# Performance work log

Hardware: AMD Instinct MI355X
Metric: run time of the kernel (lower is better)

The kernel has to match this reference:

```python
import jax, jax.numpy as jnp
import numpy as np

B, S, D, H = 4, 2048, 1024, 16
DH = D // H
NEG = -10000.0


def setup_inputs() -> dict:
    key = jax.random.key(0)
    ks = jax.random.split(key, 12)
    scale = 0.02
    inp = {
        "q": jax.random.normal(ks[0], (B, S, D), jnp.float32),
        "k": jax.random.normal(ks[1], (B, S, D), jnp.float32),
        "v": jax.random.normal(ks[2], (B, S, D), jnp.float32),
        "mask": jnp.triu(jnp.ones((S, S), jnp.bool_), k=1),  # True = masked (causal)
        "Wq": jax.random.normal(ks[3], (D, D), jnp.float32) * scale,
        "bq": jnp.zeros((D,), jnp.float32),
        "Wk": jax.random.normal(ks[4], (D, D), jnp.float32) * scale,
        "bk": jnp.zeros((D,), jnp.float32),
        "Wv": jax.random.normal(ks[5], (D, D), jnp.float32) * scale,
        "bv": jnp.zeros((D,), jnp.float32),
        "Wo": jax.random.normal(ks[6], (D, D), jnp.float32) * scale,
        "bo": jnp.zeros((D,), jnp.float32),
    }
    return inp


def _split(x):
    # [B,S,D] -> [B,H,S,DH]
    return x.reshape(B, S, H, DH).transpose(0, 2, 1, 3)


def reference(q, k, v, mask, Wq, bq, Wk, bk, Wv, bv, Wo, bo):
    # torch Linear: y = x @ W.T + b
    qh = _split(q @ Wq.T + bq)
    kh = _split(k @ Wk.T + bk)
    vh = _split(v @ Wv.T + bv)
    # scaled dot-product scores: [B,H,S,S]
    scores = jnp.einsum("bhqd,bhkd->bhqk", qh, kh) / jnp.sqrt(jnp.float32(DH))
    scores = scores + jnp.where(mask, jnp.float32(NEG), jnp.float32(0.0))
    attn = jax.nn.softmax(scores, axis=-1)  # dropout_rate=0 -> identity
    out = jnp.einsum("bhqk,bhkd->bhqd", attn, vh)
    out = out.transpose(0, 2, 1, 3).reshape(B, S, D)
    return out @ Wo.T + bo
```

## Files before the change

### kernel.cpp

```cpp
#include <hip/hip_runtime.h>
#include <hip/hip_bf16.h>


#define B_ 4
#define S_ 2048
#define D_ 1024
#define H_ 16
#define DH_ 64
#define M_ (B_*S_)
#define MASKADD (-14427.0f)
#define QSCALE  (0.180336880f)

typedef __attribute__((ext_vector_type(8)))  __bf16 bf16x8;
typedef __attribute__((ext_vector_type(8)))  unsigned short ushort8;
typedef __attribute__((ext_vector_type(4)))  float f32x4;
typedef __attribute__((ext_vector_type(16))) float f32x16;

__device__ __forceinline__ unsigned short f2bf(float f) {
  __hip_bfloat16 h = __float2bfloat16(f);
  union { __hip_bfloat16 h; unsigned short u; } c; c.h = h; return c.u;
}

__device__ __forceinline__ f32x4 mfma16(bf16x8 a, bf16x8 b, f32x4 c) {
  return __builtin_amdgcn_mfma_f32_16x16x32_bf16(a, b, c, 0, 0, 0);
}
__device__ __forceinline__ f32x16 mfma32(bf16x8 a, bf16x8 b, f32x16 c) {
  return __builtin_amdgcn_mfma_f32_32x32x16_bf16(a, b, c, 0, 0, 0);
}

__device__ __forceinline__ unsigned cvtpk(float lo, float hi) {
  unsigned r;
  asm("v_cvt_pk_bf16_f32 %0, %1, %2" : "=v"(r) : "v"(lo), "v"(hi));
  return r;
}

__device__ __forceinline__ void gld_lds16(const void* g, void* l) {
  __builtin_amdgcn_global_load_lds(
      (const __attribute__((address_space(1))) unsigned int*)g,
      (__attribute__((address_space(3))) unsigned int*)l, 16, 0, 0);
}

__global__ void cvt3_kernel(const float* __restrict__ p0, const float* __restrict__ p1,
                            const float* __restrict__ p2,
                            unsigned short* __restrict__ o0, unsigned short* __restrict__ o1,
                            unsigned short* __restrict__ o2, int n4) {
  int i = blockIdx.x * blockDim.x + threadIdx.x;
  if (i >= n4) return;
  const float* in = (blockIdx.y == 0) ? p0 : (blockIdx.y == 1 ? p1 : p2);
  unsigned short* out = (blockIdx.y == 0) ? o0 : (blockIdx.y == 1 ? o1 : o2);
  float4 f = reinterpret_cast<const float4*>(in)[i];
  ushort4 o;
  o.x = f2bf(f.x); o.y = f2bf(f.y); o.z = f2bf(f.z); o.w = f2bf(f.w);
  reinterpret_cast<ushort4*>(out)[i] = o;
}

__global__ void cvt4_kernel(const float* __restrict__ p0, const float* __restrict__ p1,
                            const float* __restrict__ p2, const float* __restrict__ p3,
                            unsigned short* __restrict__ o0, unsigned short* __restrict__ o1,
                            unsigned short* __restrict__ o2, unsigned short* __restrict__ o3,
                            int n4) {
  int i = blockIdx.x * blockDim.x + threadIdx.x;
  if (i >= n4) return;
  const float* in  = (blockIdx.y == 0) ? p0 : (blockIdx.y == 1 ? p1 : (blockIdx.y == 2 ? p2 : p3));
  unsigned short* out = (blockIdx.y == 0) ? o0 : (blockIdx.y == 1 ? o1 : (blockIdx.y == 2 ? o2 : o3));
  float4 f = reinterpret_cast<const float4*>(in)[i];
  ushort4 o;
  o.x = f2bf(f.x); o.y = f2bf(f.y); o.z = f2bf(f.z); o.w = f2bf(f.w);
  reinterpret_cast<ushort4*>(out)[i] = o;
}

__device__ __forceinline__
void gemm_body(const unsigned short* __restrict__ A, const unsigned short* __restrict__ W,
               const float* __restrict__ bias, void* __restrict__ outp,
               int mode, bool sc,
               unsigned short (*sA)[128*32], unsigned short (*sB)[128*32])
{
  const int tid  = threadIdx.x;
  const int lane = tid & 63, wid = tid >> 6;
  const int bx = blockIdx.x;
  const int j8 = bx & 7, i8 = bx >> 3;
  const int mt = j8*8 + (i8 >> 3), nt = i8 & 7;
  const int m0 = mt*128, n0 = nt*128;
  const int wr = wid >> 1, wc = wid & 1;

  f32x4 acc[4][4];
  #pragma unroll
  for (int i = 0; i < 4; ++i)
    #pragma unroll
    for (int j = 0; j < 4; ++j)
      #pragma unroll
      for (int r = 0; r < 4; ++r) acc[i][j][r] = 0.0f;

  auto stage = [&](int bufi, int kt) {
    const unsigned short* Ab = A + (size_t)m0*D_ + kt*32;
    const unsigned short* Wb = W + (size_t)n0*D_ + kt*32;
    #pragma unroll
    for (int p = 0; p < 2; ++p) {
      int r = 32*wid + 16*p + (lane >> 2);
      int c = (lane & 3) * 8;
      gld_lds16(Ab + (size_t)r*D_ + c, &sA[bufi][(32*wid + 16*p)*32]);
      gld_lds16(Wb + (size_t)r*D_ + c, &sB[bufi][(32*wid + 16*p)*32]);
    }
  };

  stage(0, 0);
  int buf = 0;
  for (int kt = 0; kt < D_/32; ++kt) {
    __syncthreads();
    if (kt + 1 < D_/32) stage(buf ^ 1, kt + 1);
    bf16x8 aF[4], bF[4];
    #pragma unroll
    for (int i = 0; i < 4; ++i)
      aF[i] = *(const bf16x8*)&sA[buf][(64*wr + 16*i + (lane & 15))*32 + (lane >> 4)*8];
    #pragma unroll
    for (int j = 0; j < 4; ++j)
      bF[j] = *(const bf16x8*)&sB[buf][(64*wc + 16*j + (lane & 15))*32 + (lane >> 4)*8];
    #pragma unroll
    for (int i = 0; i < 4; ++i)
      #pragma unroll
      for (int j = 0; j < 4; ++j)
        acc[i][j] = mfma16(aF[i], bF[j], acc[i][j]);
    buf ^= 1;
  }

  #pragma unroll
  for (int i = 0; i < 4; ++i) {
    int gr0 = m0 + 64*wr + 16*i + ((lane >> 4) << 2);
    #pragma unroll
    for (int j = 0; j < 4; ++j) {
      int gc = n0 + 64*wc + 16*j + (lane & 15);
      float bv = bias[gc];
      if (mode == 2) {
        int b = gr0 >> 11, s = gr0 & (S_ - 1);
        int hh = gc >> 6, dh = gc & (DH_ - 1);
        ushort4 o;
        o.x = f2bf(acc[i][j][0] + bv); o.y = f2bf(acc[i][j][1] + bv);
        o.z = f2bf(acc[i][j][2] + bv); o.w = f2bf(acc[i][j][3] + bv);
        *(ushort4*)&((unsigned short*)outp)[(((size_t)b*H_ + hh)*DH_ + dh)*S_ + s] = o;
      } else {
        #pragma unroll
        for (int r = 0; r < 4; ++r) {
          float v = acc[i][j][r] + bv;
          if (sc) v *= QSCALE;
          int gr = gr0 + r;
          if (mode == 0) {
            int b = gr >> 11, s = gr & (S_ - 1);
            int hh = gc >> 6, dh = gc & (DH_ - 1);
            ((unsigned short*)outp)[(((size_t)b*H_ + hh)*S_ + s)*DH_ + dh] = f2bf(v);
          } else {
            ((float*)outp)[(size_t)gr*D_ + gc] = v;
          }
        }
      }
    }
  }
}

__global__ __launch_bounds__(256, 2)
void gemm_qkv(const unsigned short* __restrict__ Aq, const unsigned short* __restrict__ Ak,
              const unsigned short* __restrict__ Av,
              const unsigned short* __restrict__ Wq_, const unsigned short* __restrict__ Wk_,
              const unsigned short* __restrict__ Wv_,
              const float* __restrict__ bq_, const float* __restrict__ bk_,
              const float* __restrict__ bv_,
              unsigned short* __restrict__ Oq, unsigned short* __restrict__ Ok,
              unsigned short* __restrict__ Ov)
{
  __shared__ unsigned short sA[2][128*32];
  __shared__ unsigned short sB[2][128*32];
  const int y = blockIdx.y;
  const unsigned short* A = (y == 0) ? Aq : (y == 1 ? Ak : Av);
  const unsigned short* W = (y == 0) ? Wq_ : (y == 1 ? Wk_ : Wv_);
  const float* bias        = (y == 0) ? bq_ : (y == 1 ? bk_ : bv_);
  unsigned short* outp     = (y == 0) ? Oq  : (y == 1 ? Ok  : Ov);
  gemm_body(A, W, bias, outp, (y == 2) ? 2 : 0, y == 0, sA, sB);
}

__global__ __launch_bounds__(256, 2)
void gemm_out(const unsigned short* __restrict__ A, const unsigned short* __restrict__ W,
              const float* __restrict__ bias, float* __restrict__ outp)
{
  __shared__ unsigned short sA[2][128*32];
  __shared__ unsigned short sB[2][128*32];
  gemm_body(A, W, bias, outp, 1, false, sA, sB);
}

__global__ __launch_bounds__(256)
void attn_kernel(const unsigned short* __restrict__ Qh, const unsigned short* __restrict__ Kh,
                 const unsigned short* __restrict__ Vt, unsigned short* __restrict__ AO)
{
  __shared__ unsigned short sK [2][64*64];
  __shared__ unsigned short sVt[2][64*64];

  const int tid = threadIdx.x, lane = tid & 63, wid = tid >> 6;
  const int l31 = lane & 31, h5 = lane >> 5;
  const int bh = blockIdx.x;
  const int chunk = 15 - (int)blockIdx.y;
  const int bb = bh >> 4, hd = bh & 15;
  const unsigned short* Qb = Qh + (size_t)bh * S_ * DH_;
  const unsigned short* Kb = Kh + (size_t)bh * S_ * DH_;
  const unsigned short* Vb = Vt + (size_t)bh * DH_ * S_;
  const int qc0 = chunk * 128;
  const int NT  = 2*chunk + 2;
  const int qw0 = qc0 + wid*32;
  const int q   = qw0 + l31;

  bf16x8 qF[4];
  #pragma unroll
  for (int c = 0; c < 4; ++c)
    qF[c] = *(const bf16x8*)(Qb + (size_t)q*DH_ + c*16 + h5*8);

  f32x16 zz;
  #pragma unroll
  for (int r = 0; r < 16; ++r) zz[r] = 0.0f;
  f32x16 accO0 = zz, accO1 = zz;
  float lsum = 0.0f;

  auto stageK = [&](int bufi, int t) {
    #pragma unroll
    for (int p = 0; p < 2; ++p) {
      int ch = 2*wid + p;
      int row = ch*8 + (lane >> 3);
      int cbs = ((lane & 7) * 16) ^ ((row & 7) << 4);
      gld_lds16(Kb + (size_t)(t*64 + row)*DH_ + (cbs >> 1), &sK[bufi][ch*512]);
    }
  };
  auto stageV = [&](int bufi, int t) {
    #pragma unroll
    for (int p = 0; p < 2; ++p) {
      int ch = 2*wid + p;
      int row = ch*8 + (lane >> 3);
      int cbs = ((lane & 7) * 16) ^ ((row & 7) << 4);
      gld_lds16(Vb + (size_t)row*S_ + t*64 + (cbs >> 1), &sVt[bufi][ch*512]);
    }
  };

  stageK(0, 0);
  stageV(0, 0);

  int buf = 0;
  for (int t = 0; t < NT; ++t) {
    __syncthreads();
    if (t + 1 < NT) { stageK(buf ^ 1, t + 1); stageV(buf ^ 1, t + 1); }

    #pragma unroll
    for (int sub = 0; sub < 2; ++sub) {
      const int kv0 = t*64 + sub*32;
      if (kv0 > qw0 + 31) continue;
      const bool dodiag = (kv0 + 31 > qw0);

      f32x16 st = zz;
      __builtin_amdgcn_s_setprio(1);
      #pragma unroll
      for (int c = 0; c < 4; ++c) {
        int row = sub*32 + l31;
        const char* base = (const char*)&sK[buf][0] + row*128;
        bf16x8 kf = *(const bf16x8*)(base + ((32*c + 16*h5) ^ ((row & 7) << 4)));
        st = mfma32(kf, qF[c], st);
      }
      __builtin_amdgcn_s_setprio(0);

      #pragma unroll
      for (int r = 0; r < 16; ++r) {
        float x = st[r];
        if (dodiag) {
          int kv = kv0 + (r & 3) + 8*(r >> 2) + 4*h5;
          if (kv > q) x += MASKADD;
        }
        x = __builtin_amdgcn_exp2f(x);
        st[r] = x;
        lsum += x;
      }

      #pragma unroll
      for (int hh = 0; hh < 2; ++hh) {
        union { unsigned u[4]; bf16x8 v; } pb;
        pb.u[0] = cvtpk(st[8*hh+0], st[8*hh+1]);
        pb.u[1] = cvtpk(st[8*hh+2], st[8*hh+3]);
        pb.u[2] = cvtpk(st[8*hh+4], st[8*hh+5]);
        pb.u[3] = cvtpk(st[8*hh+6], st[8*hh+7]);

        __builtin_amdgcn_s_setprio(1);
        #pragma unroll
        for (int dh = 0; dh < 2; ++dh) {
          int row = dh*32 + l31;
          const char* base = (const char*)&sVt[buf][0] + row*128;
          int sw = (row & 7) << 4;
          int X = 64*sub + 32*hh + 8*h5;
          union { uint2 g[2]; bf16x8 v; } vv;
          vv.g[0] = *(const uint2*)(base + ((X)      ^ sw));
          vv.g[1] = *(const uint2*)(base + ((X + 16) ^ sw));
          if (dh == 0) accO0 = mfma32(vv.v, pb.v, accO0);
          else         accO1 = mfma32(vv.v, pb.v, accO1);
        }
        __builtin_amdgcn_s_setprio(0);
      }
    }
    buf ^= 1;
  }

  float lt = lsum + __shfl_xor(lsum, 32, 64);
  float inv = 1.0f / lt;
  unsigned short* ao = AO + ((size_t)bb*S_ + q)*D_ + hd*DH_;
  #pragma unroll
  for (int dh = 0; dh < 2; ++dh) {
    const f32x16 A = dh ? accO1 : accO0;
    #pragma unroll
    for (int rq = 0; rq < 4; ++rq) {
      ushort4 o;
      o.x = f2bf(A[4*rq+0] * inv);
      o.y = f2bf(A[4*rq+1] * inv);
      o.z = f2bf(A[4*rq+2] * inv);
      o.w = f2bf(A[4*rq+3] * inv);
      int dbase = dh*32 + 8*rq + 4*h5;
      *(ushort4*)&ao[dbase] = o;
    }
  }
}

extern "C" void kernel_launch(void* const* d_in, const int* in_sizes, int n_in,
                              void* d_out, int out_size, void* d_ws, size_t ws_size,
                              hipStream_t stream)
{
  const float* q  = (const float*)d_in[0];
  const float* k  = (const float*)d_in[1];
  const float* v  = (const float*)d_in[2];
  const float* Wq = (const float*)d_in[4];
  const float* bq = (const float*)d_in[5];
  const float* Wk = (const float*)d_in[6];
  const float* bk = (const float*)d_in[7];
  const float* Wv = (const float*)d_in[8];
  const float* bv = (const float*)d_in[9];
  const float* Wo = (const float*)d_in[10];
  const float* bo = (const float*)d_in[11];

  unsigned short* ws = (unsigned short*)d_ws;
  const size_t MD = (size_t)M_ * D_;
  const size_t DD = (size_t)D_ * D_;
  unsigned short* qb  = ws;
  unsigned short* kb  = qb  + MD;
  unsigned short* vb  = kb  + MD;
  unsigned short* Wqb = vb  + MD;
  unsigned short* Wkb = Wqb + DD;
  unsigned short* Wvb = Wkb + DD;
  unsigned short* Wob = Wvb + DD;
  unsigned short* Qhb = Wob + DD;
  unsigned short* Khb = Qhb + MD;
  unsigned short* Vtb = Khb + MD;
  unsigned short* AOb = Vtb + MD;

  cvt3_kernel<<<dim3((int)(MD/4/256), 3), 256, 0, stream>>>(q, k, v, qb, kb, vb, (int)(MD/4));
  cvt4_kernel<<<dim3((int)(DD/4/256), 4), 256, 0, stream>>>(Wq, Wk, Wv, Wo, Wqb, Wkb, Wvb, Wob, (int)(DD/4));

  gemm_qkv<<<dim3(512, 3), 256, 0, stream>>>(qb, kb, vb, Wqb, Wkb, Wvb,
                                             bq, bk, bv, Qhb, Khb, Vtb);

  attn_kernel<<<dim3(64, 16), 256, 0, stream>>>(Qhb, Khb, Vtb, AOb);

  gemm_out<<<512, 256, 0, stream>>>(AOb, Wob, bo, (float*)d_out);
}
```

Before: 193.0 us.

## Fuse fp32-to-bf16 activation conversion into QKV GEMM A-tile loading

Removes the separate conversion kernel for q/k/v. The QKV GEMM now reads fp32 activations directly into registers, converts them to bf16, and writes them to shared memory, with the next tile's global loads issued before the MFMAs so they overlap compute. This avoids writing and re-reading three bf16 activation copies and saves a kernel launch. In exchange, the GEMM's A-tile traffic is twice as wide, register pressure rises, and the async global-to-LDS path is replaced by register staging for A.

```diff
diff --git a/kernel.cpp b/kernel.cpp
--- a/kernel.cpp
+++ b/kernel.cpp
@@ -38,20 +38,6 @@
   __builtin_amdgcn_global_load_lds(
       (const __attribute__((address_space(1))) unsigned int*)g,
       (__attribute__((address_space(3))) unsigned int*)l, 16, 0, 0);
-}
-
-__global__ void cvt3_kernel(const float* __restrict__ p0, const float* __restrict__ p1,
-                            const float* __restrict__ p2,
-                            unsigned short* __restrict__ o0, unsigned short* __restrict__ o1,
-                            unsigned short* __restrict__ o2, int n4) {
-  int i = blockIdx.x * blockDim.x + threadIdx.x;
-  if (i >= n4) return;
-  const float* in = (blockIdx.y == 0) ? p0 : (blockIdx.y == 1 ? p1 : p2);
-  unsigned short* out = (blockIdx.y == 0) ? o0 : (blockIdx.y == 1 ? o1 : o2);
-  float4 f = reinterpret_cast<const float4*>(in)[i];
-  ushort4 o;
-  o.x = f2bf(f.x); o.y = f2bf(f.y); o.z = f2bf(f.z); o.w = f2bf(f.w);
-  reinterpret_cast<ushort4*>(out)[i] = o;
 }
 
 __global__ void cvt4_kernel(const float* __restrict__ p0, const float* __restrict__ p1,
@@ -69,8 +55,9 @@
   reinterpret_cast<ushort4*>(out)[i] = o;
 }
 
+template<bool F32A>
 __device__ __forceinline__
-void gemm_body(const unsigned short* __restrict__ A, const unsigned short* __restrict__ W,
+void gemm_body(const void* __restrict__ Ap, const unsigned short* __restrict__ W,
                const float* __restrict__ bias, void* __restrict__ outp,
                int mode, bool sc,
                unsigned short (*sA)[128*32], unsigned short (*sB)[128*32])
@@ -83,6 +70,9 @@
   const int m0 = mt*128, n0 = nt*128;
   const int wr = wid >> 1, wc = wid & 1;
 
+  const float* A32 = (const float*)Ap;
+  const unsigned short* A16 = (const unsigned short*)Ap;
+
   f32x4 acc[4][4];
   #pragma unroll
   for (int i = 0; i < 4; ++i)
@@ -91,23 +81,55 @@
       #pragma unroll
       for (int r = 0; r < 4; ++r) acc[i][j][r] = 0.0f;
 
-  auto stage = [&](int bufi, int kt) {
-    const unsigned short* Ab = A + (size_t)m0*D_ + kt*32;
+  auto stageB = [&](int bufi, int kt) {
     const unsigned short* Wb = W + (size_t)n0*D_ + kt*32;
+    #pragma unroll
+    for (int p = 0; p < 2; ++p) {
+      int r = 32*wid + 16*p + (lane >> 2);
+      int c = (lane & 3) * 8;
+      gld_lds16(Wb + (size_t)r*D_ + c, &sB[bufi][(32*wid + 16*p)*32]);
+    }
+  };
+  auto stageA16 = [&](int bufi, int kt) {
+    const unsigned short* Ab = A16 + (size_t)m0*D_ + kt*32;
     #pragma unroll
     for (int p = 0; p < 2; ++p) {
       int r = 32*wid + 16*p + (lane >> 2);
       int c = (lane & 3) * 8;
       gld_lds16(Ab + (size_t)r*D_ + c, &sA[bufi][(32*wid + 16*p)*32]);
-      gld_lds16(Wb + (size_t)r*D_ + c, &sB[bufi][(32*wid + 16*p)*32]);
-    }
-  };
-
-  stage(0, 0);
+    }
+  };
+
+  f32x4 fr[4];
+  auto loadA32 = [&](int kt) {
+    const float* p = A32 + (size_t)(m0 + (tid >> 1))*D_ + kt*32 + (tid & 1)*16;
+    fr[0] = *(const f32x4*)(p);
+    fr[1] = *(const f32x4*)(p + 4);
+    fr[2] = *(const f32x4*)(p + 8);
+    fr[3] = *(const f32x4*)(p + 12);
+  };
+  auto writeA32 = [&](int bufi) {
+    ushort8 o0, o1;
+    #pragma unroll
+    for (int j = 0; j < 4; ++j) {
+      o0[j]   = f2bf(fr[0][j]);
+      o0[4+j] = f2bf(fr[1][j]);
+      o1[j]   = f2bf(fr[2][j]);
+      o1[4+j] = f2bf(fr[3][j]);
+    }
+    unsigned short* dst = &sA[bufi][(tid >> 1)*32 + (tid & 1)*16];
+    *(ushort8*)dst       = o0;
+    *(ushort8*)(dst + 8) = o1;
+  };
+
+  if (F32A) { loadA32(0); writeA32(0); }
+  else      { stageA16(0, 0); }
+  stageB(0, 0);
+
+  const int NK = D_/32;
   int buf = 0;
-  for (int kt = 0; kt < D_/32; ++kt) {
+  for (int kt = 0; kt < NK; ++kt) {
     __syncthreads();
-    if (kt + 1 < D_/32) stage(buf ^ 1, kt + 1);
     bf16x8 aF[4], bF[4];
     #pragma unroll
     for (int i = 0; i < 4; ++i)
@@ -115,11 +137,20 @@
     #pragma unroll
     for (int j = 0; j < 4; ++j)
       bF[j] = *(const bf16x8*)&sB[buf][(64*wc + 16*j + (lane & 15))*32 + (lane >> 4)*8];
+
+    if (kt + 1 < NK) {
+      if (F32A) loadA32(kt + 1);
+      else      stageA16(buf ^ 1, kt + 1);
+      stageB(buf ^ 1, kt + 1);
+    }
+
     #pragma unroll
     for (int i = 0; i < 4; ++i)
       #pragma unroll
       for (int j = 0; j < 4; ++j)
         acc[i][j] = mfma16(aF[i], bF[j], acc[i][j]);
+
+    if (F32A && kt + 1 < NK) writeA32(buf ^ 1);
     buf ^= 1;
   }
 
@@ -157,8 +188,8 @@
 }
 
 __global__ __launch_bounds__(256, 2)
-void gemm_qkv(const unsigned short* __restrict__ Aq, const unsigned short* __restrict__ Ak,
-              const unsigned short* __restrict__ Av,
+void gemm_qkv(const float* __restrict__ Aq, const float* __restrict__ Ak,
+              const float* __restrict__ Av,
               const unsigned short* __restrict__ Wq_, const unsigned short* __restrict__ Wk_,
               const unsigned short* __restrict__ Wv_,
               const float* __restrict__ bq_, const float* __restrict__ bk_,
@@ -169,11 +200,11 @@
   __shared__ unsigned short sA[2][128*32];
   __shared__ unsigned short sB[2][128*32];
   const int y = blockIdx.y;
-  const unsigned short* A = (y == 0) ? Aq : (y == 1 ? Ak : Av);
+  const float* A = (y == 0) ? Aq : (y == 1 ? Ak : Av);
   const unsigned short* W = (y == 0) ? Wq_ : (y == 1 ? Wk_ : Wv_);
   const float* bias        = (y == 0) ? bq_ : (y == 1 ? bk_ : bv_);
   unsigned short* outp     = (y == 0) ? Oq  : (y == 1 ? Ok  : Ov);
-  gemm_body(A, W, bias, outp, (y == 2) ? 2 : 0, y == 0, sA, sB);
+  gemm_body<true>(A, W, bias, outp, (y == 2) ? 2 : 0, y == 0, sA, sB);
 }
 
 __global__ __launch_bounds__(256, 2)
@@ -182,7 +213,7 @@
 {
   __shared__ unsigned short sA[2][128*32];
   __shared__ unsigned short sB[2][128*32];
-  gemm_body(A, W, bias, outp, 1, false, sA, sB);
+  gemm_body<false>(A, W, bias, outp, 1, false, sA, sB);
 }
 
 __global__ __launch_bounds__(256)
@@ -337,10 +368,7 @@
   unsigned short* ws = (unsigned short*)d_ws;
   const size_t MD = (size_t)M_ * D_;
   const size_t DD = (size_t)D_ * D_;
-  unsigned short* qb  = ws;
-  unsigned short* kb  = qb  + MD;
-  unsigned short* vb  = kb  + MD;
-  unsigned short* Wqb = vb  + MD;
+  unsigned short* Wqb = ws;
   unsigned short* Wkb = Wqb + DD;
   unsigned short* Wvb = Wkb + DD;
   unsigned short* Wob = Wvb + DD;
@@ -349,10 +377,9 @@
   unsigned short* Vtb = Khb + MD;
   unsigned short* AOb = Vtb + MD;
 
-  cvt3_kernel<<<dim3((int)(MD/4/256), 3), 256, 0, stream>>>(q, k, v, qb, kb, vb, (int)(MD/4));
   cvt4_kernel<<<dim3((int)(DD/4/256), 4), 256, 0, stream>>>(Wq, Wk, Wv, Wo, Wqb, Wkb, Wvb, Wob, (int)(DD/4));
 
-  gemm_qkv<<<dim3(512, 3), 256, 0, stream>>>(qb, kb, vb, Wqb, Wkb, Wvb,
+  gemm_qkv<<<dim3(512, 3), 256, 0, stream>>>(q, k, v, Wqb, Wkb, Wvb,
                                              bq, bk, bv, Qhb, Khb, Vtb);
 
   attn_kernel<<<dim3(64, 16), 256, 0, stream>>>(Qhb, Khb, Vtb, AOb);
```

After: 190.7 us. No clear change (-1.2%).
